# Performance work log

Hardware: AMD Instinct MI355X
Metric: run time of the kernel (lower is better)

Reference implementation:

```python
import jax, jax.numpy as jnp
import numpy as np

# Shapes / hyperparams (match init_kwargs and input_specs)
B, CIN, COUT, H, W = 8, 128, 128, 64, 64
K, S, P, D = 3, 1, 1, 1
KK = K * K
EPS = 1e-5  # BatchNorm eps


def setup_inputs() -> dict:
    key = jax.random.key(0)
    ks = jax.random.split(key, 4)
    x = jax.random.normal(ks[0], (B, CIN, H, W), jnp.float32)
    # small offset weights so predicted offsets stay O(1) pixels
    w_off = jax.random.normal(ks[1], (2 * KK, CIN, K, K), jnp.float32) * 0.01
    w_def = jax.random.normal(ks[2], (COUT, CIN, K, K), jnp.float32) * (1.0 / np.sqrt(CIN * KK))
    b_def = jax.random.normal(ks[3], (COUT,), jnp.float32) * 0.01
    gamma = jnp.ones((COUT,), jnp.float32)
    beta = jnp.zeros((COUT,), jnp.float32)
    return dict(x=x, w_off=w_off, w_def=w_def, b_def=b_def, gamma=gamma, beta=beta)


def _bilinear_gather(x, ys, xs):
    """x: [B,C,H,W]; ys/xs: [B,KK,Ho,Wo] float coords -> [B,C,KK,Ho,Wo].
    Zero padding outside the image (torchvision DeformConv2d semantics)."""
    Bb, C, Hh, Ww = x.shape
    y0 = jnp.floor(ys)
    x0 = jnp.floor(xs)
    wy = ys - y0
    wx = xs - x0
    xf = x.reshape(Bb, C, Hh * Ww)

    def gather(yi, xi, w):
        valid = (yi >= 0) & (yi < Hh) & (xi >= 0) & (xi < Ww)
        idx = (jnp.clip(yi, 0, Hh - 1) * Ww + jnp.clip(xi, 0, Ww - 1)).astype(jnp.int32)
        g = jnp.take_along_axis(xf, idx.reshape(Bb, 1, -1), axis=2)  # [B,C,KK*Ho*Wo]
        g = g.reshape(Bb, C, *idx.shape[1:])  # [B,C,KK,Ho,Wo]
        return g * (w * valid)[:, None]

    return (gather(y0, x0, (1 - wy) * (1 - wx))
            + gather(y0, x0 + 1, (1 - wy) * wx)
            + gather(y0 + 1, x0, wy * (1 - wx))
            + gather(y0 + 1, x0 + 1, wy * wx))


def _forward(x, w_off, w_def, b_def, gamma, beta):
    # 1) offset prediction: standard conv, no bias
    offset = jax.lax.conv_general_dilated(
        x, w_off, window_strides=(S, S), padding=((P, P), (P, P)),
        rhs_dilation=(D, D), dimension_numbers=('NCHW', 'OIHW', 'NCHW'))
    Ho, Wo = offset.shape[2], offset.shape[3]
    off = offset.reshape(B, KK, 2, Ho, Wo)  # (dy, dx) pairs per kernel loc
    dy, dx = off[:, :, 0], off[:, :, 1]

    # 2) deformable sampling coordinates
    ky = (jnp.arange(KK) // K).astype(jnp.float32) * D  # kernel row offset
    kx = (jnp.arange(KK) % K).astype(jnp.float32) * D   # kernel col offset
    base_y = (jnp.arange(Ho) * S - P).astype(jnp.float32)
    base_x = (jnp.arange(Wo) * S - P).astype(jnp.float32)
    ys = base_y[None, None, :, None] + ky[None, :, None, None] + dy  # [B,KK,Ho,Wo]
    xs = base_x[None, None, None, :] + kx[None, :, None, None] + dx

    sampled = _bilinear_gather(x, ys, xs)  # [B,CIN,KK,Ho,Wo]

    # 3) per-kernel-location weighted accumulation (implicit GEMM) + bias
    out = jnp.einsum('bckhw,ock->bohw', sampled, w_def.reshape(COUT, CIN, KK))
    out = out + b_def[None, :, None, None]

    # 4) BatchNorm2d (training mode: batch statistics) + SiLU
    mean = out.mean(axis=(0, 2, 3))
    var = out.var(axis=(0, 2, 3))
    scale = gamma / jnp.sqrt(var + EPS)
    out = (out - mean[None, :, None, None]) * scale[None, :, None, None] + beta[None, :, None, None]
    return out * jax.nn.sigmoid(out)  # SiLU


def reference(x, w_off, w_def, b_def, gamma, beta):
    return _forward(x, w_off, w_def, b_def, gamma, beta)
```

## Files before the change

### kernel.cpp

```cpp
#include <hip/hip_runtime.h>
#include <math.h>

#define CIN   128
#define COUT  128
#define KKT   9
#define NSTAT 32768.0f

typedef __attribute__((ext_vector_type(8))) short bf16x8;
typedef __attribute__((ext_vector_type(4))) float f32x4;

__device__ inline unsigned short f2bf(float f) {
    union { float f; unsigned u; } v; v.f = f;
    unsigned r = v.u + 0x7fffu + ((v.u >> 16) & 1u);
    return (unsigned short)(r >> 16);
}
__device__ inline float bflo(unsigned u) { union { unsigned u; float f; } v; v.u = u << 16; return v.f; }
__device__ inline float bfhi(unsigned u) { union { unsigned u; float f; } v; v.u = u & 0xffff0000u; return v.f; }

#define FAST_BARRIER() asm volatile("s_waitcnt lgkmcnt(0)\n\ts_barrier" ::: "memory")


__global__ __launch_bounds__(512) void prep_xt_k(const float* __restrict__ x,
                                                 unsigned* __restrict__ xt) {
    __shared__ float lt[128][65];
    const int by = blockIdx.x;
    const int b = by >> 6, y = by & 63;
    const int t = threadIdx.x, l = t & 63, g8 = t >> 6;
    const float* xb = x + (b * 128) * 4096 + y * 64;
#pragma unroll
    for (int pass = 0; pass < 16; pass++) {
        int c = pass * 8 + g8;
        lt[c][l] = xb[c * 4096 + l];
    }
    __syncthreads();
    unsigned* xo = xt + (by * 64) * 64;
#pragma unroll
    for (int pass = 0; pass < 8; pass++) {
        int w = pass * 8 + g8;
        float f0 = lt[2 * l][w], f1 = lt[2 * l + 1][w];
        xo[w * 64 + l] = (unsigned)f2bf(f0) | ((unsigned)f2bf(f1) << 16);
    }
}

__global__ __launch_bounds__(256) void repack_w_k(const float* __restrict__ w_def,
                                                  const float* __restrict__ w_off,
                                                  unsigned short* __restrict__ wb,
                                                  unsigned short* __restrict__ wob,
                                                  float* __restrict__ sums) {
    int i = blockIdx.x * 256 + threadIdx.x;
    if (i < 147456) {
        int oc = i / 1152, r = i - oc * 1152, kt = r >> 7, c = r & 127;
        wb[i] = f2bf(w_def[(oc * 128 + c) * 9 + kt]);
    } else if (i < 147456 + 36864) {
        int j = i - 147456;
        int ocp = j / 1152, r = j - ocp * 1152, kt = r >> 7, c = r & 127;
        wob[j] = (ocp < 18) ? f2bf(w_off[(ocp * 128 + c) * 9 + kt]) : (unsigned short)0;
    } else if (i < 147456 + 36864 + 256) {
        sums[i - 147456 - 36864] = 0.f;
    }
}

#define RB 51200
__global__ __launch_bounds__(512, 4) void deform_main_k(const unsigned* __restrict__ xt,
                                                        const unsigned short* __restrict__ wb,
                                                        const unsigned short* __restrict__ wob,
                                                        const float* __restrict__ b_def,
                                                        float* __restrict__ out,
                                                        float* __restrict__ sums,
                                                        float* __restrict__ sumsq) {
    __shared__ __align__(16) unsigned char smem[RB + 4608 + 1024];
    unsigned short* xrow = (unsigned short*)smem;
    int*            tab  = (int*)smem;
    unsigned short* samp0 = (unsigned short*)(smem + 18432);
    unsigned short* samp1 = (unsigned short*)(smem + 34816);
    float* offl = (float*)(smem + RB);
    float* stat = (float*)(smem + RB + 4608);

    const int t    = threadIdx.x;
    const int bh   = blockIdx.x;
    const int b    = bh >> 6;
    const int j_   = bh & 63;
    const int h    = ((j_ & 7) << 3) | (j_ >> 3);
    const int lane = t & 63;
    const int wv   = __builtin_amdgcn_readfirstlane(t >> 6);
    const int quad = lane >> 4, lo = lane & 15;
    const int l    = lane;
    const int g    = lane >> 2;

    if (t < 256) stat[t] = 0.f;

    const unsigned* xtb = xt + b * 262144;

    for (int p = wv; p < 198; p += 8) {
        int r = p / 66, xi = p - r * 66;
        int y = h + r - 1, x = xi - 1;
        unsigned u = 0;
        if ((unsigned)y < 64u && (unsigned)x < 64u) u = xtb[(y * 64 + x) * 64 + l];
        ((unsigned*)xrow)[(r * 66 + xi) * 64 + ((g ^ (xi & 15)) << 2) + (l & 3)] = u;
    }
    __syncthreads();

    {
        const int mt = wv >> 2, nt = wv & 3;
        f32x4 ao = {0.f, 0.f, 0.f, 0.f};
        const unsigned short* wrow = wob + (mt * 16 + lo) * 1152 + quad * 8;
        for (int kt = 0; kt < 9; kt++) {
            int ky = kt / 3, kx = kt - ky * 3;
            int xi = nt * 16 + lo + kx;
#pragma unroll
            for (int ch = 0; ch < 4; ch++) {
                int gg = ch * 4 + quad;
                bf16x8 af = *(const bf16x8*)(wrow + kt * 128 + ch * 32);
                bf16x8 bf = *(const bf16x8*)(xrow + (ky * 66 + xi) * 128 + ((gg ^ (xi & 15)) << 3));
                ao = __builtin_amdgcn_mfma_f32_16x16x32_bf16(af, bf, ao, 0, 0, 0);
            }
        }
        __syncthreads();
#pragma unroll
        for (int r = 0; r < 4; r++) {
            int oc = mt * 16 + quad * 4 + r;
            if (oc < 18) offl[oc * 64 + nt * 16 + lo] = ao[r];
        }
    }
    __syncthreads();

    for (int i = t; i < KKT * 64; i += 512) {
        int k = i >> 6, w2 = i & 63;
        float dy = offl[(2 * k) * 64 + w2];
        float dx = offl[(2 * k + 1) * 64 + w2];
        int ky = k / 3, kx = k - ky * 3;
        float ys = (float)(h - 1 + ky) + dy;
        float xs = (float)(w2 - 1 + kx) + dx;
        float y0f = floorf(ys), x0f = floorf(xs);
        float wyf = ys - y0f, wxf = xs - x0f;
        int iy0 = (int)y0f, ix0 = (int)x0f;
        int cy0 = min(max(iy0, 0), 63), cy1 = min(max(iy0 + 1, 0), 63);
        int px  = min(max(ix0, 0), 63), px2 = min(max(ix0 + 1, 0), 63);
        float wy0 = (iy0 >= 0 && iy0 < 64) ? (1.f - wyf) : 0.f;
        float wy1 = (iy0 + 1 >= 0 && iy0 + 1 < 64) ? wyf : 0.f;
        float wa  = (ix0 >= 0 && ix0 < 64) ? (1.f - wxf) : 0.f;
        float wbv = (ix0 + 1 >= 0 && ix0 + 1 < 64) ? wxf : 0.f;
        int base = i * 8;
        tab[base + 0] = (cy0 * 64 + px ) * 64;
        tab[base + 1] = (cy0 * 64 + px2) * 64;
        tab[base + 2] = (cy1 * 64 + px ) * 64;
        tab[base + 3] = (cy1 * 64 + px2) * 64;
        ((float*)tab)[base + 4] = wy0;
        ((float*)tab)[base + 5] = wy1;
        ((float*)tab)[base + 6] = wa;
        ((float*)tab)[base + 7] = wbv;
    }
    __syncthreads();

    const int m0 = wv >> 1, n0 = wv & 1;
    f32x4 acc[2][2];
#pragma unroll
    for (int i = 0; i < 2; i++)
#pragma unroll
        for (int j = 0; j < 2; j++)
#pragma unroll
            for (int r = 0; r < 4; r++) acc[i][j][r] = 0.f;

    const unsigned short* wrow0 = wb + (2 * m0 * 16 + lo) * 1152 + quad * 8;
    const unsigned short* wrow1 = wrow0 + 16 * 1152;

    for (int kt = 0; kt < KKT; kt++) {
        bf16x8 af0[4], af1[4];
#pragma unroll
        for (int ch = 0; ch < 4; ch++) {
            af0[ch] = *(const bf16x8*)(wrow0 + kt * 128 + ch * 32);
            af1[ch] = *(const bf16x8*)(wrow1 + kt * 128 + ch * 32);
        }
        unsigned* sb = (unsigned*)((kt & 1) ? samp1 : samp0);
#pragma unroll
        for (int i = 0; i < 8; i++) {
            int w = wv * 8 + i;
            int bse = (kt * 64 + w) * 8;
            int4   ta = *(const int4*)&tab[bse];
            float4 tw = *(const float4*)&tab[bse + 4];
            unsigned u00 = xtb[ta.x + l];
            unsigned u01 = xtb[ta.y + l];
            unsigned u10 = xtb[ta.z + l];
            unsigned u11 = xtb[ta.w + l];
            float e = tw.x * (tw.z * bflo(u00) + tw.w * bflo(u01)) +
                      tw.y * (tw.z * bflo(u10) + tw.w * bflo(u11));
            float o = tw.x * (tw.z * bfhi(u00) + tw.w * bfhi(u01)) +
                      tw.y * (tw.z * bfhi(u10) + tw.w * bfhi(u11));
            sb[w * 64 + ((g ^ (w & 15)) << 2) + (l & 3)] =
                (unsigned)f2bf(e) | ((unsigned)f2bf(o) << 16);
        }
        FAST_BARRIER();
        const unsigned short* sbs = (kt & 1) ? samp1 : samp0;
#pragma unroll
        for (int ch = 0; ch < 4; ch++) {
            int gg = ch * 4 + quad;
            int r0 = (2 * n0 + 0) * 16 + lo, r1 = (2 * n0 + 1) * 16 + lo;
            bf16x8 bf0 = *(const bf16x8*)(sbs + r0 * 128 + ((gg ^ lo) << 3));
            bf16x8 bf1 = *(const bf16x8*)(sbs + r1 * 128 + ((gg ^ lo) << 3));
            acc[0][0] = __builtin_amdgcn_mfma_f32_16x16x32_bf16(af0[ch], bf0, acc[0][0], 0, 0, 0);
            acc[0][1] = __builtin_amdgcn_mfma_f32_16x16x32_bf16(af0[ch], bf1, acc[0][1], 0, 0, 0);
            acc[1][0] = __builtin_amdgcn_mfma_f32_16x16x32_bf16(af1[ch], bf0, acc[1][0], 0, 0, 0);
            acc[1][1] = __builtin_amdgcn_mfma_f32_16x16x32_bf16(af1[ch], bf1, acc[1][1], 0, 0, 0);
        }
    }

    float* ob = out + b * COUT * 4096 + h * 64;
#pragma unroll
    for (int mt2 = 0; mt2 < 2; mt2++) {
        int ocb = (2 * m0 + mt2) * 16 + quad * 4;
#pragma unroll
        for (int r = 0; r < 4; r++) {
            int oc = ocb + r;
            float bia = b_def[oc];
            float ssum = 0.f, qsum = 0.f;
#pragma unroll
            for (int nt2 = 0; nt2 < 2; nt2++) {
                int w_ = (2 * n0 + nt2) * 16 + lo;
                float v = acc[mt2][nt2][r] + bia;
                ob[oc * 4096 + w_] = v;
                ssum += v; qsum += v * v;
            }
#pragma unroll
            for (int d = 1; d < 16; d <<= 1) {
                ssum += __shfl_xor(ssum, d, 64);
                qsum += __shfl_xor(qsum, d, 64);
            }
            if (lo == 0) { atomicAdd(&stat[oc], ssum); atomicAdd(&stat[128 + oc], qsum); }
        }
    }
    __syncthreads();
    if (t < 256) {
        float* gp = (t < 128) ? (sums + t) : (sumsq + (t - 128));
        atomicAdd(gp, stat[t]);
    }
}

__global__ __launch_bounds__(256) void bn_silu_k(float* __restrict__ out,
                                                 const float* __restrict__ sums,
                                                 const float* __restrict__ sumsq,
                                                 const float* __restrict__ gamma,
                                                 const float* __restrict__ beta) {
    __shared__ float sc_s[128], sh_s[128];
    int t = threadIdx.x;
    if (t < 128) {
        const float invN = 1.f / NSTAT;
        float m = sums[t] * invN;
        float v = fmaf(-m, m, sumsq[t] * invN);
        float sc = gamma[t] * rsqrtf(v + 1e-5f);
        sc_s[t] = sc;
        sh_s[t] = beta[t] - m * sc;
    }
    __syncthreads();
    int i = blockIdx.x * 256 + t;
    float4 v = ((float4*)out)[i];
    int oc = (i >> 10) & 127;
    float sc = sc_s[oc], sh = sh_s[oc];
    float z0 = v.x * sc + sh;
    float z1 = v.y * sc + sh;
    float z2 = v.z * sc + sh;
    float z3 = v.w * sc + sh;
    v.x = z0 / (1.f + __expf(-z0));
    v.y = z1 / (1.f + __expf(-z1));
    v.z = z2 / (1.f + __expf(-z2));
    v.w = z3 / (1.f + __expf(-z3));
    ((float4*)out)[i] = v;
}

extern "C" void kernel_launch(void* const* d_in, const int* in_sizes, int n_in,
                              void* d_out, int out_size, void* d_ws, size_t ws_size,
                              hipStream_t stream) {
    const float* x     = (const float*)d_in[0];
    const float* w_off = (const float*)d_in[1];
    const float* w_def = (const float*)d_in[2];
    const float* b_def = (const float*)d_in[3];
    const float* gamma = (const float*)d_in[4];
    const float* beta  = (const float*)d_in[5];
    float* out = (float*)d_out;

    unsigned*       xt   = (unsigned*)d_ws;
    unsigned short* wb   = (unsigned short*)((char*)d_ws + 16777216);
    unsigned short* wob  = (unsigned short*)((char*)d_ws + 17072128);
    float*          sums = (float*)((char*)d_ws + 17145856);
    float*          sumsq = sums + 128;

    prep_xt_k<<<512, 512, 0, stream>>>(x, xt);
    repack_w_k<<<721, 256, 0, stream>>>(w_def, w_off, wb, wob, sums);
    deform_main_k<<<512, 512, 0, stream>>>(xt, wb, wob, b_def, out, sums, sumsq);
    bn_silu_k<<<4096, 256, 0, stream>>>(out, sums, sumsq, gamma, beta);
}
```

Before: 168.7 us.

## Prefetch next tap's bilinear gathers into registers and merge prep kernels

The main loop now issues the global gathers for the next kernel tap into registers before the barrier and MFMA work of the current tap, so gather latency overlaps with compute. Bilinear weights are precombined into four corner weights, the blend uses FMAs, and packing uses a hardware bf16 convert. The two prep kernels are merged into one launch, and the halo-load loop is unrolled. This raises register pressure (32 extra live values per thread), which can hurt occupancy under the 4-blocks launch bound.

```diff
diff --git a/kernel.cpp b/kernel.cpp
--- a/kernel.cpp
+++ b/kernel.cpp
@@ -17,46 +17,48 @@
 __device__ inline float bflo(unsigned u) { union { unsigned u; float f; } v; v.u = u << 16; return v.f; }
 __device__ inline float bfhi(unsigned u) { union { unsigned u; float f; } v; v.u = u & 0xffff0000u; return v.f; }
 
-#define FAST_BARRIER() asm volatile("s_waitcnt lgkmcnt(0)\n\ts_barrier" ::: "memory")
-
-
-__global__ __launch_bounds__(512) void prep_xt_k(const float* __restrict__ x,
-                                                 unsigned* __restrict__ xt) {
-    __shared__ float lt[128][65];
-    const int by = blockIdx.x;
-    const int b = by >> 6, y = by & 63;
-    const int t = threadIdx.x, l = t & 63, g8 = t >> 6;
-    const float* xb = x + (b * 128) * 4096 + y * 64;
-#pragma unroll
-    for (int pass = 0; pass < 16; pass++) {
-        int c = pass * 8 + g8;
-        lt[c][l] = xb[c * 4096 + l];
-    }
-    __syncthreads();
-    unsigned* xo = xt + (by * 64) * 64;
-#pragma unroll
-    for (int pass = 0; pass < 8; pass++) {
-        int w = pass * 8 + g8;
-        float f0 = lt[2 * l][w], f1 = lt[2 * l + 1][w];
-        xo[w * 64 + l] = (unsigned)f2bf(f0) | ((unsigned)f2bf(f1) << 16);
-    }
-}
-
-__global__ __launch_bounds__(256) void repack_w_k(const float* __restrict__ w_def,
+#define PUB_BARRIER() do { asm volatile("s_waitcnt lgkmcnt(0)" ::: "memory"); \
+                           __builtin_amdgcn_s_barrier(); } while (0)
+
+
+__global__ __launch_bounds__(512) void prep_all_k(const float* __restrict__ x,
+                                                  unsigned* __restrict__ xt,
+                                                  const float* __restrict__ w_def,
                                                   const float* __restrict__ w_off,
                                                   unsigned short* __restrict__ wb,
                                                   unsigned short* __restrict__ wob,
                                                   float* __restrict__ sums) {
-    int i = blockIdx.x * 256 + threadIdx.x;
-    if (i < 147456) {
-        int oc = i / 1152, r = i - oc * 1152, kt = r >> 7, c = r & 127;
-        wb[i] = f2bf(w_def[(oc * 128 + c) * 9 + kt]);
-    } else if (i < 147456 + 36864) {
-        int j = i - 147456;
-        int ocp = j / 1152, r = j - ocp * 1152, kt = r >> 7, c = r & 127;
-        wob[j] = (ocp < 18) ? f2bf(w_off[(ocp * 128 + c) * 9 + kt]) : (unsigned short)0;
-    } else if (i < 147456 + 36864 + 256) {
-        sums[i - 147456 - 36864] = 0.f;
+    __shared__ float lt[128][65];
+    const int bb = blockIdx.x;
+    if (bb < 512) {
+        const int b = bb >> 6, y = bb & 63;
+        const int t = threadIdx.x, l = t & 63, g8 = t >> 6;
+        const float* xb = x + (b * 128) * 4096 + y * 64;
+#pragma unroll
+        for (int pass = 0; pass < 16; pass++) {
+            int c = pass * 8 + g8;
+            lt[c][l] = xb[c * 4096 + l];
+        }
+        __syncthreads();
+        unsigned* xo = xt + (bb * 64) * 64;
+#pragma unroll
+        for (int pass = 0; pass < 8; pass++) {
+            int w = pass * 8 + g8;
+            float f0 = lt[2 * l][w], f1 = lt[2 * l + 1][w];
+            xo[w * 64 + l] = (unsigned)f2bf(f0) | ((unsigned)f2bf(f1) << 16);
+        }
+    } else {
+        int i = (bb - 512) * 512 + threadIdx.x;
+        if (i < 147456) {
+            int oc = i / 1152, r = i - oc * 1152, kt = r >> 7, c = r & 127;
+            wb[i] = f2bf(w_def[(oc * 128 + c) * 9 + kt]);
+        } else if (i < 147456 + 36864) {
+            int j = i - 147456;
+            int ocp = j / 1152, r = j - ocp * 1152, kt = r >> 7, c = r & 127;
+            wob[j] = (ocp < 18) ? f2bf(w_off[(ocp * 128 + c) * 9 + kt]) : (unsigned short)0;
+        } else if (i < 147456 + 36864 + 256) {
+            sums[i - 147456 - 36864] = 0.f;
+        }
     }
 }
 
@@ -91,12 +93,16 @@
 
     const unsigned* xtb = xt + b * 262144;
 
-    for (int p = wv; p < 198; p += 8) {
-        int r = p / 66, xi = p - r * 66;
-        int y = h + r - 1, x = xi - 1;
-        unsigned u = 0;
-        if ((unsigned)y < 64u && (unsigned)x < 64u) u = xtb[(y * 64 + x) * 64 + l];
-        ((unsigned*)xrow)[(r * 66 + xi) * 64 + ((g ^ (xi & 15)) << 2) + (l & 3)] = u;
+#pragma unroll
+    for (int it = 0; it < 25; it++) {
+        int p = wv + it * 8;
+        if (p < 198) {
+            int r = p / 66, xi = p - r * 66;
+            int y = h + r - 1, x = xi - 1;
+            unsigned u = 0;
+            if ((unsigned)y < 64u && (unsigned)x < 64u) u = xtb[(y * 64 + x) * 64 + l];
+            ((unsigned*)xrow)[(r * 66 + xi) * 64 + ((g ^ (xi & 15)) << 2) + (l & 3)] = u;
+        }
     }
     __syncthreads();
 
@@ -145,14 +151,15 @@
         tab[base + 1] = (cy0 * 64 + px2) * 64;
         tab[base + 2] = (cy1 * 64 + px ) * 64;
         tab[base + 3] = (cy1 * 64 + px2) * 64;
-        ((float*)tab)[base + 4] = wy0;
-        ((float*)tab)[base + 5] = wy1;
-        ((float*)tab)[base + 6] = wa;
-        ((float*)tab)[base + 7] = wbv;
+        ((float*)tab)[base + 4] = wy0 * wa;
+        ((float*)tab)[base + 5] = wy0 * wbv;
+        ((float*)tab)[base + 6] = wy1 * wa;
+        ((float*)tab)[base + 7] = wy1 * wbv;
     }
     __syncthreads();
 
     const int m0 = wv >> 1, n0 = wv & 1;
+    const int w0 = wv * 8;
     f32x4 acc[2][2];
 #pragma unroll
     for (int i = 0; i < 2; i++)
@@ -164,32 +171,48 @@
     const unsigned short* wrow0 = wb + (2 * m0 * 16 + lo) * 1152 + quad * 8;
     const unsigned short* wrow1 = wrow0 + 16 * 1152;
 
+    unsigned u0[8], u1[8], u2[8], u3[8];
+
+#pragma unroll
+    for (int i = 0; i < 8; i++) {
+        const int4 a = *(const int4*)&tab[(w0 + i) * 8];
+        u0[i] = xtb[a.x + l]; u1[i] = xtb[a.y + l];
+        u2[i] = xtb[a.z + l]; u3[i] = xtb[a.w + l];
+    }
+
     for (int kt = 0; kt < KKT; kt++) {
+        unsigned* sb = (unsigned*)((kt & 1) ? samp1 : samp0);
+#pragma unroll
+        for (int i = 0; i < 8; i++) {
+            const float4 tw = *(const float4*)&tab[(kt * 64 + w0 + i) * 8 + 4];
+            float e = tw.x * bflo(u0[i]);
+            e = fmaf(tw.y, bflo(u1[i]), e);
+            e = fmaf(tw.z, bflo(u2[i]), e);
+            e = fmaf(tw.w, bflo(u3[i]), e);
+            float o = tw.x * bfhi(u0[i]);
+            o = fmaf(tw.y, bfhi(u1[i]), o);
+            o = fmaf(tw.z, bfhi(u2[i]), o);
+            o = fmaf(tw.w, bfhi(u3[i]), o);
+            unsigned pk;
+            asm("v_cvt_pk_bf16_f32 %0, %1, %2" : "=v"(pk) : "v"(e), "v"(o));
+            int w = w0 + i;
+            sb[w * 64 + ((g ^ (w & 15)) << 2) + (l & 3)] = pk;
+        }
         bf16x8 af0[4], af1[4];
 #pragma unroll
         for (int ch = 0; ch < 4; ch++) {
             af0[ch] = *(const bf16x8*)(wrow0 + kt * 128 + ch * 32);
             af1[ch] = *(const bf16x8*)(wrow1 + kt * 128 + ch * 32);
         }
-        unsigned* sb = (unsigned*)((kt & 1) ? samp1 : samp0);
-#pragma unroll
-        for (int i = 0; i < 8; i++) {
-            int w = wv * 8 + i;
-            int bse = (kt * 64 + w) * 8;
-            int4   ta = *(const int4*)&tab[bse];
-            float4 tw = *(const float4*)&tab[bse + 4];
-            unsigned u00 = xtb[ta.x + l];
-            unsigned u01 = xtb[ta.y + l];
-            unsigned u10 = xtb[ta.z + l];
-            unsigned u11 = xtb[ta.w + l];
-            float e = tw.x * (tw.z * bflo(u00) + tw.w * bflo(u01)) +
-                      tw.y * (tw.z * bflo(u10) + tw.w * bflo(u11));
-            float o = tw.x * (tw.z * bfhi(u00) + tw.w * bfhi(u01)) +
-                      tw.y * (tw.z * bfhi(u10) + tw.w * bfhi(u11));
-            sb[w * 64 + ((g ^ (w & 15)) << 2) + (l & 3)] =
-                (unsigned)f2bf(e) | ((unsigned)f2bf(o) << 16);
-        }
-        FAST_BARRIER();
+        if (kt < KKT - 1) {
+#pragma unroll
+            for (int i = 0; i < 8; i++) {
+                const int4 a = *(const int4*)&tab[((kt + 1) * 64 + w0 + i) * 8];
+                u0[i] = xtb[a.x + l]; u1[i] = xtb[a.y + l];
+                u2[i] = xtb[a.z + l]; u3[i] = xtb[a.w + l];
+            }
+        }
+        PUB_BARRIER();
         const unsigned short* sbs = (kt & 1) ? samp1 : samp0;
 #pragma unroll
         for (int ch = 0; ch < 4; ch++) {
@@ -283,8 +306,7 @@
     float*          sums = (float*)((char*)d_ws + 17145856);
     float*          sumsq = sums + 128;
 
-    prep_xt_k<<<512, 512, 0, stream>>>(x, xt);
-    repack_w_k<<<721, 256, 0, stream>>>(w_def, w_off, wb, wob, sums);
+    prep_all_k<<<873, 512, 0, stream>>>(x, xt, w_def, w_off, wb, wob, sums);
     deform_main_k<<<512, 512, 0, stream>>>(xt, wb, wob, b_def, out, sums, sumsq);
     bn_silu_k<<<4096, 256, 0, stream>>>(out, sums, sumsq, gamma, beta);
 }
```

Result: faster. 158.2 us (-6.2%).
